# Kernel tuning notes

Hardware: AMD Instinct MI355X
Metric: run time of the kernel (lower is better)

The kernel has to match this reference:

```python
import jax, jax.numpy as jnp
import numpy as np

N_HIDDEN_LAYERS = 9  # 32->32 middle layers (plus input 1->32 and output 32->1)
HID = 32
SLOPE = 0.01  # LeakyReLU negative_slope


def leaky_relu(x):
    return jnp.where(x >= 0, x, SLOPE * x)


def setup_inputs() -> dict:
    key = jax.random.key(0)
    ks = jax.random.split(key, 8)
    N = 1048576
    x = jax.random.normal(ks[0], (N,), dtype=jnp.float32)
    # PyTorch Linear init: U(-1/sqrt(fan_in), 1/sqrt(fan_in))
    def u(k, shape, fan_in):
        b = 1.0 / np.sqrt(fan_in)
        return jax.random.uniform(k, shape, jnp.float32, -b, b)
    W_in = u(ks[1], (1, HID), 1)
    b_in = u(ks[2], (HID,), 1)
    W_hid = u(ks[3], (N_HIDDEN_LAYERS, HID, HID), HID)
    b_hid = u(ks[4], (N_HIDDEN_LAYERS, HID), HID)
    W_out = u(ks[5], (HID, 1), HID)
    b_out = u(ks[6], (1,), HID)
    return {"x": x, "W_in": W_in, "b_in": b_in, "W_hid": W_hid,
            "b_hid": b_hid, "W_out": W_out, "b_out": b_out}


def reference(x, W_in, b_in, W_hid, b_hid, W_out, b_out):
    N = x.shape[0]
    h = x[:, None]  # [N, 1], mirrors x.reshape(N, 1)
    h = leaky_relu(h @ W_in + b_in)  # [N, 32]
    def step(h, wb):
        W, b = wb
        return leaky_relu(h @ W + b), None
    h, _ = jax.lax.scan(step, h, (W_hid, b_hid))
    out = h @ W_out + b_out  # [N, 1]
    return out.reshape(1, N)
```

## Files before the change

kernel.cpp:

```cpp
#include <hip/hip_runtime.h>

#define NLAYERS 9
#define HID 32
#define SLOPE 0.01f

typedef _Float16 v2h __attribute__((ext_vector_type(2)));
typedef _Float16 v8h __attribute__((ext_vector_type(8)));
typedef float v16f __attribute__((ext_vector_type(16)));

#define NCHAIN 4

union U8 { v8h v; v2h p[4]; };
struct B4 { v2h a, b, c, d; };

__device__ __forceinline__ v2h pk_cvt(float a, float b) {
    return __builtin_bit_cast(v2h, __builtin_amdgcn_cvt_pkrtz(a, b));
}
__device__ __forceinline__ v2h leaky2(v2h t, v2h s) {
    return __builtin_elementwise_max(t, t * s);
}
__device__ __forceinline__ int qmap(int k) {
    int c = k >> 4, h = (k >> 3) & 1, t = k & 7;
    return 16 * c + 4 * h + (t & 3) + 8 * (t >> 2);
}
__device__ __forceinline__ int rmap(int reg, int h) {
    return (reg & 3) + 8 * (reg >> 2) + 4 * h;
}

__global__ __launch_bounds__(256, 2) void mlp_mfma_kernel(
    const float* __restrict__ x,
    const float* __restrict__ W_in,
    const float* __restrict__ b_in,
    const float* __restrict__ W_hid,
    const float* __restrict__ b_hid,
    const float* __restrict__ W_out,
    const float* __restrict__ b_out,
    float* __restrict__ out, int N)
{
    __shared__ __align__(16) v2h bias_sh[NLAYERS][2][8];
    for (int t = threadIdx.x; t < NLAYERS * 16; t += blockDim.x) {
        int l = t >> 4, r = t & 15, h = r >> 3, j = r & 7;
        bias_sh[l][h][j] = v2h{(_Float16)b_hid[l * HID + rmap(2 * j, h)],
                               (_Float16)b_hid[l * HID + rmap(2 * j + 1, h)]};
    }
    __syncthreads();

    const int lane = threadIdx.x & 63;
    const int half = lane >> 5;
    const int m    = lane & 31;

    v8h alo[NLAYERS], ahi[NLAYERS];
#pragma unroll
    for (int l = 0; l < NLAYERS; ++l) {
        const float* Wl = W_hid + l * HID * HID;
#pragma unroll
        for (int j = 0; j < 8; ++j) {
            alo[l][j] = (_Float16)Wl[qmap(8 * half + j) * HID + m];
            ahi[l][j] = (_Float16)Wl[qmap(16 + 8 * half + j) * HID + m];
        }
    }
    v2h win2[8], bin2[8], wout2[8];
#pragma unroll
    for (int u = 0; u < 8; ++u) {
        int i0 = 2 * u, i1 = 2 * u + 1;
        int d0 = qmap(((i0 >> 3) << 4) + 8 * half + (i0 & 7));
        int d1 = qmap(((i1 >> 3) << 4) + 8 * half + (i1 & 7));
        win2[u]  = v2h{(_Float16)W_in[d0],  (_Float16)W_in[d1]};
        bin2[u]  = v2h{(_Float16)b_in[d0],  (_Float16)b_in[d1]};
        wout2[u] = v2h{(_Float16)W_out[d0], (_Float16)W_out[d1]};
    }
    const float bo = b_out[0];
    const v2h slope2 = v2h{(_Float16)SLOPE, (_Float16)SLOPE};
    const v16f z16 = {};

    const int nwaves = (gridDim.x * blockDim.x) >> 6;
    const int wid    = (blockIdx.x * blockDim.x + threadIdx.x) >> 6;
    const int niter  = (N + NCHAIN * 32 - 1) / (NCHAIN * 32);

    float xc[NCHAIN] = {0.0f, 0.0f, 0.0f, 0.0f};
    if (wid < niter) {
#pragma unroll
        for (int c = 0; c < NCHAIN; ++c) {
            int idx = wid * (NCHAIN * 32) + c * 32 + m;
            xc[c] = (idx < N) ? x[idx] : 0.0f;
        }
    }

    for (int it = wid; it < niter; it += nwaves) {
        float xn[NCHAIN] = {0.0f, 0.0f, 0.0f, 0.0f};
        {
            int nit = it + nwaves;
            if (nit < niter) {
#pragma unroll
                for (int c = 0; c < NCHAIN; ++c) {
                    int idx = nit * (NCHAIN * 32) + c * 32 + m;
                    xn[c] = (idx < N) ? x[idx] : 0.0f;
                }
            }
        }

        U8 clo[NCHAIN], chi[NCHAIN];
#pragma unroll
        for (int c = 0; c < NCHAIN; ++c) {
            _Float16 xh = (_Float16)xc[c];
            v2h x2 = v2h{xh, xh};
#pragma unroll
            for (int u = 0; u < 4; ++u) {
                clo[c].p[u] = leaky2(x2 * win2[u] + bin2[u], slope2);
                chi[c].p[u] = leaky2(x2 * win2[4 + u] + bin2[4 + u], slope2);
            }
        }

#pragma unroll
        for (int l = 0; l < NLAYERS; ++l) {
            B4 q0 = __builtin_bit_cast(B4, ((const uint4*)&bias_sh[l][half][0])[0]);
            B4 q1 = __builtin_bit_cast(B4, ((const uint4*)&bias_sh[l][half][4])[0]);

            v16f a[NCHAIN];
#pragma unroll
            for (int c = 0; c < NCHAIN; ++c)
                a[c] = __builtin_amdgcn_mfma_f32_32x32x16_f16(alo[l], clo[c].v, z16, 0, 0, 0);
#pragma unroll
            for (int c = 0; c < NCHAIN; ++c)
                a[c] = __builtin_amdgcn_mfma_f32_32x32x16_f16(ahi[l], chi[c].v, a[c], 0, 0, 0);

            v2h bl[8] = {q0.a, q0.b, q0.c, q0.d, q1.a, q1.b, q1.c, q1.d};
#pragma unroll
            for (int c = 0; c < NCHAIN; ++c) {
#pragma unroll
                for (int u = 0; u < 4; ++u) {
                    clo[c].p[u] = leaky2(pk_cvt(a[c][2 * u], a[c][2 * u + 1]) + bl[u], slope2);
                    chi[c].p[u] = leaky2(pk_cvt(a[c][8 + 2 * u], a[c][8 + 2 * u + 1]) + bl[4 + u], slope2);
                }
            }
        }

#pragma unroll
        for (int c = 0; c < NCHAIN; ++c) {
            float p = 0.0f;
#pragma unroll
            for (int u = 0; u < 4; ++u) {
                p = fmaf((float)clo[c].p[u][0], (float)wout2[u][0], p);
                p = fmaf((float)clo[c].p[u][1], (float)wout2[u][1], p);
                p = fmaf((float)chi[c].p[u][0], (float)wout2[4 + u][0], p);
                p = fmaf((float)chi[c].p[u][1], (float)wout2[4 + u][1], p);
            }
            float o = p + __shfl_xor(p, 32, 64) + bo;
            int idx = it * (NCHAIN * 32) + c * 32 + m;
            if (half == (c >> 1) && idx < N) out[idx] = o;
        }

#pragma unroll
        for (int c = 0; c < NCHAIN; ++c) xc[c] = xn[c];
    }
}

extern "C" void kernel_launch(void* const* d_in, const int* in_sizes, int n_in,
                              void* d_out, int out_size, void* d_ws, size_t ws_size,
                              hipStream_t stream) {
    const float* x     = (const float*)d_in[0];
    const float* W_in  = (const float*)d_in[1];
    const float* b_in  = (const float*)d_in[2];
    const float* W_hid = (const float*)d_in[3];
    const float* b_hid = (const float*)d_in[4];
    const float* W_out = (const float*)d_in[5];
    const float* b_out = (const float*)d_in[6];
    float* out = (float*)d_out;

    int N = in_sizes[0];
    dim3 block(256);
    dim3 grid(512);
    mlp_mfma_kernel<<<grid, block, 0, stream>>>(x, W_in, b_in, W_hid, b_hid,
                                                W_out, b_out, out, N);
}
```

Measured before the change: 96.22 us.

## Move MLP weights from registers to LDS and double occupancy

Hidden-layer weight fragments and input/output vectors now live in shared memory and are read per layer, instead of being held in registers for the whole kernel. The bias is loaded in fp32 and used as the MFMA accumulator initialiser, which removes the separate fp16 bias add. Chains are processed in pairs to cut live accumulators. Launch bounds move to 4 blocks per CU and the grid doubles, aiming for more waves to hide MFMA and conversion latency, at the cost of LDS reads on every layer.

```diff
diff --git a/kernel.cpp b/kernel.cpp
--- a/kernel.cpp
+++ b/kernel.cpp
@@ -11,7 +11,7 @@
 #define NCHAIN 4
 
 union U8 { v8h v; v2h p[4]; };
-struct B4 { v2h a, b, c, d; };
+struct U16 { v2h p[8]; };
 
 __device__ __forceinline__ v2h pk_cvt(float a, float b) {
     return __builtin_bit_cast(v2h, __builtin_amdgcn_cvt_pkrtz(a, b));
@@ -27,7 +27,7 @@
     return (reg & 3) + 8 * (reg >> 2) + 4 * h;
 }
 
-__global__ __launch_bounds__(256, 2) void mlp_mfma_kernel(
+__global__ __launch_bounds__(256, 4) void mlp_mfma_kernel(
     const float* __restrict__ x,
     const float* __restrict__ W_in,
     const float* __restrict__ b_in,
@@ -37,44 +37,50 @@
     const float* __restrict__ b_out,
     float* __restrict__ out, int N)
 {
-    __shared__ __align__(16) v2h bias_sh[NLAYERS][2][8];
-    for (int t = threadIdx.x; t < NLAYERS * 16; t += blockDim.x) {
-        int l = t >> 4, r = t & 15, h = r >> 3, j = r & 7;
-        bias_sh[l][h][j] = v2h{(_Float16)b_hid[l * HID + rmap(2 * j, h)],
-                               (_Float16)b_hid[l * HID + rmap(2 * j + 1, h)]};
+    __shared__ __align__(16) _Float16 wlo_sh[NLAYERS][64][8];
+    __shared__ __align__(16) _Float16 whi_sh[NLAYERS][64][8];
+    __shared__ __align__(64) float bc_sh[NLAYERS][2][16];
+    __shared__ __align__(32) v2h win_sh[2][8];
+    __shared__ __align__(32) v2h bin_sh[2][8];
+    __shared__ __align__(32) v2h wout_sh[2][8];
+
+    const int tid = threadIdx.x;
+    for (int t = tid; t < NLAYERS * 64; t += blockDim.x) {
+        int l = t >> 6, ln = t & 63, hf = (ln >> 5) & 1, mm = ln & 31;
+        const float* Wl = W_hid + l * HID * HID;
+        v8h lo, hi;
+#pragma unroll
+        for (int j = 0; j < 8; ++j) {
+            lo[j] = (_Float16)Wl[qmap(8 * hf + j) * HID + mm];
+            hi[j] = (_Float16)Wl[qmap(16 + 8 * hf + j) * HID + mm];
+        }
+        *(v8h*)&wlo_sh[l][ln][0] = lo;
+        *(v8h*)&whi_sh[l][ln][0] = hi;
+    }
+    for (int t = tid; t < NLAYERS * 32; t += blockDim.x) {
+        int l = t >> 5, r = t & 31, hf = r >> 4, reg = r & 15;
+        bc_sh[l][hf][reg] = b_hid[l * HID + rmap(reg, hf)];
+    }
+    if (tid < 16) {
+        int hf = tid >> 3, u = tid & 7;
+        int i0 = 2 * u, i1 = 2 * u + 1;
+        int d0 = qmap(((i0 >> 3) << 4) + 8 * hf + (i0 & 7));
+        int d1 = qmap(((i1 >> 3) << 4) + 8 * hf + (i1 & 7));
+        win_sh[hf][u]  = v2h{(_Float16)W_in[d0],  (_Float16)W_in[d1]};
+        bin_sh[hf][u]  = v2h{(_Float16)b_in[d0],  (_Float16)b_in[d1]};
+        wout_sh[hf][u] = v2h{(_Float16)W_out[d0], (_Float16)W_out[d1]};
     }
     __syncthreads();
 
-    const int lane = threadIdx.x & 63;
+    const int lane = tid & 63;
     const int half = lane >> 5;
     const int m    = lane & 31;
 
-    v8h alo[NLAYERS], ahi[NLAYERS];
-#pragma unroll
-    for (int l = 0; l < NLAYERS; ++l) {
-        const float* Wl = W_hid + l * HID * HID;
-#pragma unroll
-        for (int j = 0; j < 8; ++j) {
-            alo[l][j] = (_Float16)Wl[qmap(8 * half + j) * HID + m];
-            ahi[l][j] = (_Float16)Wl[qmap(16 + 8 * half + j) * HID + m];
-        }
-    }
-    v2h win2[8], bin2[8], wout2[8];
-#pragma unroll
-    for (int u = 0; u < 8; ++u) {
-        int i0 = 2 * u, i1 = 2 * u + 1;
-        int d0 = qmap(((i0 >> 3) << 4) + 8 * half + (i0 & 7));
-        int d1 = qmap(((i1 >> 3) << 4) + 8 * half + (i1 & 7));
-        win2[u]  = v2h{(_Float16)W_in[d0],  (_Float16)W_in[d1]};
-        bin2[u]  = v2h{(_Float16)b_in[d0],  (_Float16)b_in[d1]};
-        wout2[u] = v2h{(_Float16)W_out[d0], (_Float16)W_out[d1]};
-    }
     const float bo = b_out[0];
     const v2h slope2 = v2h{(_Float16)SLOPE, (_Float16)SLOPE};
-    const v16f z16 = {};
 
     const int nwaves = (gridDim.x * blockDim.x) >> 6;
-    const int wid    = (blockIdx.x * blockDim.x + threadIdx.x) >> 6;
+    const int wid    = (blockIdx.x * blockDim.x + tid) >> 6;
     const int niter  = (N + NCHAIN * 32 - 1) / (NCHAIN * 32);
 
     float xc[NCHAIN] = {0.0f, 0.0f, 0.0f, 0.0f};
@@ -100,54 +106,59 @@
         }
 
         U8 clo[NCHAIN], chi[NCHAIN];
+        {
+            U16 wi = *(const U16*)&win_sh[half][0];
+            U16 bi = *(const U16*)&bin_sh[half][0];
 #pragma unroll
-        for (int c = 0; c < NCHAIN; ++c) {
-            _Float16 xh = (_Float16)xc[c];
-            v2h x2 = v2h{xh, xh};
+            for (int c = 0; c < NCHAIN; ++c) {
+                _Float16 xh = (_Float16)xc[c];
+                v2h x2 = v2h{xh, xh};
 #pragma unroll
-            for (int u = 0; u < 4; ++u) {
-                clo[c].p[u] = leaky2(x2 * win2[u] + bin2[u], slope2);
-                chi[c].p[u] = leaky2(x2 * win2[4 + u] + bin2[4 + u], slope2);
+                for (int u = 0; u < 4; ++u) {
+                    clo[c].p[u] = leaky2(x2 * wi.p[u] + bi.p[u], slope2);
+                    chi[c].p[u] = leaky2(x2 * wi.p[4 + u] + bi.p[4 + u], slope2);
+                }
             }
         }
 
 #pragma unroll
         for (int l = 0; l < NLAYERS; ++l) {
-            B4 q0 = __builtin_bit_cast(B4, ((const uint4*)&bias_sh[l][half][0])[0]);
-            B4 q1 = __builtin_bit_cast(B4, ((const uint4*)&bias_sh[l][half][4])[0]);
-
-            v16f a[NCHAIN];
+            v8h wlo = *(const v8h*)&wlo_sh[l][lane][0];
+            v8h whi = *(const v8h*)&whi_sh[l][lane][0];
+            v16f bc = *(const v16f*)&bc_sh[l][half][0];
 #pragma unroll
-            for (int c = 0; c < NCHAIN; ++c)
-                a[c] = __builtin_amdgcn_mfma_f32_32x32x16_f16(alo[l], clo[c].v, z16, 0, 0, 0);
-#pragma unroll
-            for (int c = 0; c < NCHAIN; ++c)
-                a[c] = __builtin_amdgcn_mfma_f32_32x32x16_f16(ahi[l], chi[c].v, a[c], 0, 0, 0);
-
-            v2h bl[8] = {q0.a, q0.b, q0.c, q0.d, q1.a, q1.b, q1.c, q1.d};
-#pragma unroll
-            for (int c = 0; c < NCHAIN; ++c) {
+            for (int g = 0; g < NCHAIN / 2; ++g) {
+                const int c0 = 2 * g, c1 = 2 * g + 1;
+                v16f a0 = __builtin_amdgcn_mfma_f32_32x32x16_f16(wlo, clo[c0].v, bc, 0, 0, 0);
+                v16f a1 = __builtin_amdgcn_mfma_f32_32x32x16_f16(wlo, clo[c1].v, bc, 0, 0, 0);
+                a0 = __builtin_amdgcn_mfma_f32_32x32x16_f16(whi, chi[c0].v, a0, 0, 0, 0);
+                a1 = __builtin_amdgcn_mfma_f32_32x32x16_f16(whi, chi[c1].v, a1, 0, 0, 0);
 #pragma unroll
                 for (int u = 0; u < 4; ++u) {
-                    clo[c].p[u] = leaky2(pk_cvt(a[c][2 * u], a[c][2 * u + 1]) + bl[u], slope2);
-                    chi[c].p[u] = leaky2(pk_cvt(a[c][8 + 2 * u], a[c][8 + 2 * u + 1]) + bl[4 + u], slope2);
+                    clo[c0].p[u] = leaky2(pk_cvt(a0[2 * u], a0[2 * u + 1]), slope2);
+                    chi[c0].p[u] = leaky2(pk_cvt(a0[8 + 2 * u], a0[8 + 2 * u + 1]), slope2);
+                    clo[c1].p[u] = leaky2(pk_cvt(a1[2 * u], a1[2 * u + 1]), slope2);
+                    chi[c1].p[u] = leaky2(pk_cvt(a1[8 + 2 * u], a1[8 + 2 * u + 1]), slope2);
                 }
             }
         }
 
+        {
+            U16 wo = *(const U16*)&wout_sh[half][0];
 #pragma unroll
-        for (int c = 0; c < NCHAIN; ++c) {
-            float p = 0.0f;
+            for (int c = 0; c < NCHAIN; ++c) {
+                float p = 0.0f;
 #pragma unroll
-            for (int u = 0; u < 4; ++u) {
-                p = fmaf((float)clo[c].p[u][0], (float)wout2[u][0], p);
-                p = fmaf((float)clo[c].p[u][1], (float)wout2[u][1], p);
-                p = fmaf((float)chi[c].p[u][0], (float)wout2[4 + u][0], p);
-                p = fmaf((float)chi[c].p[u][1], (float)wout2[4 + u][1], p);
+                for (int u = 0; u < 4; ++u) {
+                    p = fmaf((float)clo[c].p[u][0], (float)wo.p[u][0], p);
+                    p = fmaf((float)clo[c].p[u][1], (float)wo.p[u][1], p);
+                    p = fmaf((float)chi[c].p[u][0], (float)wo.p[4 + u][0], p);
+                    p = fmaf((float)chi[c].p[u][1], (float)wo.p[4 + u][1], p);
+                }
+                float o = p + __shfl_xor(p, 32, 64) + bo;
+                int idx = it * (NCHAIN * 32) + c * 32 + m;
+                if (half == (c >> 1) && idx < N) out[idx] = o;
             }
-            float o = p + __shfl_xor(p, 32, 64) + bo;
-            int idx = it * (NCHAIN * 32) + c * 32 + m;
-            if (half == (c >> 1) && idx < N) out[idx] = o;
         }
 
 #pragma unroll
@@ -169,7 +180,7 @@
 
     int N = in_sizes[0];
     dim3 block(256);
-    dim3 grid(512);
+    dim3 grid(1024);
     mlp_mfma_kernel<<<grid, block, 0, stream>>>(x, W_in, b_in, W_hid, b_hid,
                                                 W_out, b_out, out, N);
 }
```

New measurement: 201.5 us. 109% more time.
